# Optimization experiments

Measured on AMD Instinct MI355X. Metric: run time of the kernel, lower is better.

## Reference

```python
import jax, jax.numpy as jnp
import numpy as np

SEQ_LENGTH = 4096
D_MODEL = 2048


def setup_inputs() -> dict:
    key = jax.random.key(0)
    x = jax.random.randint(key, (32, SEQ_LENGTH), 0, 2048)  # [B, S] token ids
    return {"x": x}


def reference(x):
    batch_size = x.shape[0]
    n = 10000.0
    pos = jnp.arange(SEQ_LENGTH, dtype=jnp.float32)[:, None]          # [S, 1]
    i = jnp.arange(D_MODEL // 2, dtype=jnp.float32)[None, :]          # [1, D/2]
    theta = pos / jnp.power(n, (2.0 * i) / D_MODEL)                   # [S, D/2]
    # interleave: even dims = sin, odd dims = cos
    pe = jnp.stack([jnp.sin(theta), jnp.cos(theta)], axis=-1)
    pe = pe.reshape(SEQ_LENGTH, D_MODEL)                              # [S, D]
    return jnp.broadcast_to(pe[None, :, :], (batch_size, SEQ_LENGTH, D_MODEL))
```

## Files before the change

kernel.cpp:

```cpp
#include <hip/hip_runtime.h>
#include <math.h>

#define SEQ_LENGTH 4096
#define D_MODEL   2048
#define BATCH     32
#define TABLE_F4  (SEQ_LENGTH * D_MODEL / 4)
#define TOTAL_F4  (BATCH * TABLE_F4)
#define IT        8

typedef float f4 __attribute__((ext_vector_type(4)));

__global__ __launch_bounds__(256) void PositionalEncoding_54915451847173_kernel(
    float* __restrict__ out) {
    const int base = blockIdx.x * (256 * IT) + threadIdx.x;

    const float c      = -(2.0f / (float)D_MODEL) * 13.28771237954945f;
    const float inv2pi = 0.15915494309189535f;

    #pragma unroll
    for (int it = 0; it < IT; ++it) {
        const int u  = base + it * 256;
        const int t  = u & (TABLE_F4 - 1);
        const int jj = t & (D_MODEL / 4 - 1);
        const int s  = t >> 9;

        const float pos = (float)s;
        const float f0 = __builtin_amdgcn_exp2f(c * (float)(2 * jj));
        const float f1 = __builtin_amdgcn_exp2f(c * (float)(2 * jj + 1));

        const float r0 = __builtin_amdgcn_fractf(pos * (f0 * inv2pi));
        const float r1 = __builtin_amdgcn_fractf(pos * (f1 * inv2pi));

        f4 v;
        v.x = __builtin_amdgcn_sinf(r0);
        v.y = __builtin_amdgcn_cosf(r0);
        v.z = __builtin_amdgcn_sinf(r1);
        v.w = __builtin_amdgcn_cosf(r1);

        ((f4*)out)[u] = v;
    }
}

extern "C" void kernel_launch(void* const* d_in, const int* in_sizes, int n_in,
                              void* d_out, int out_size, void* d_ws, size_t ws_size,
                              hipStream_t stream) {
    (void)d_in; (void)in_sizes; (void)n_in; (void)d_ws; (void)ws_size; (void)out_size;
    float* out = (float*)d_out;
    const int grid = TOTAL_F4 / (256 * IT);
    PositionalEncoding_54915451847173_kernel<<<grid, 256, 0, stream>>>(out);
}
```

Before: 197.2 us.

## Compute each table entry once and stream it to all batch copies

Switches to a persistent grid-stride layout of 2048 blocks. Each thread computes the frequencies for one column once and the sin/cos values for four sequence positions, then writes those four vectors repeatedly across the whole output with a fixed stride. The stride is chosen so the same four values recur across all 32 batch copies. This drops the redundant per-element transcendental work, leaving a purely write-bound store loop. The cost is fewer threads in flight and a serial, non-unrolled store loop per thread.

```diff
diff --git a/kernel.cpp b/kernel.cpp
--- a/kernel.cpp
+++ b/kernel.cpp
@@ -6,38 +6,44 @@
 #define BATCH     32
 #define TABLE_F4  (SEQ_LENGTH * D_MODEL / 4)
 #define TOTAL_F4  (BATCH * TABLE_F4)
-#define IT        8
+#define GRID      2048
+#define STRIDE_F4 (GRID * 256)
+#define NITER     (TOTAL_F4 / STRIDE_F4)
 
 typedef float f4 __attribute__((ext_vector_type(4)));
 
 __global__ __launch_bounds__(256) void PositionalEncoding_54915451847173_kernel(
     float* __restrict__ out) {
-    const int base = blockIdx.x * (256 * IT) + threadIdx.x;
+    const int base = blockIdx.x * 256 + threadIdx.x;
+    const int jj   = base & (D_MODEL / 4 - 1);
+    const int s0   = base >> 9;
 
     const float c      = -(2.0f / (float)D_MODEL) * 13.28771237954945f;
     const float inv2pi = 0.15915494309189535f;
+    const float w0 = __builtin_amdgcn_exp2f(c * (float)(2 * jj)) * inv2pi;
+    const float w1 = __builtin_amdgcn_exp2f(c * (float)(2 * jj + 1)) * inv2pi;
 
+    f4 v[4];
     #pragma unroll
-    for (int it = 0; it < IT; ++it) {
-        const int u  = base + it * 256;
-        const int t  = u & (TABLE_F4 - 1);
-        const int jj = t & (D_MODEL / 4 - 1);
-        const int s  = t >> 9;
+    for (int q = 0; q < 4; ++q) {
+        const float pos = (float)(s0 + 1024 * q);
+        const float r0 = __builtin_amdgcn_fractf(pos * w0);
+        const float r1 = __builtin_amdgcn_fractf(pos * w1);
+        f4 t;
+        t.x = __builtin_amdgcn_sinf(r0);
+        t.y = __builtin_amdgcn_cosf(r0);
+        t.z = __builtin_amdgcn_sinf(r1);
+        t.w = __builtin_amdgcn_cosf(r1);
+        v[q] = t;
+    }
 
-        const float pos = (float)s;
-        const float f0 = __builtin_amdgcn_exp2f(c * (float)(2 * jj));
-        const float f1 = __builtin_amdgcn_exp2f(c * (float)(2 * jj + 1));
-
-        const float r0 = __builtin_amdgcn_fractf(pos * (f0 * inv2pi));
-        const float r1 = __builtin_amdgcn_fractf(pos * (f1 * inv2pi));
-
-        f4 v;
-        v.x = __builtin_amdgcn_sinf(r0);
-        v.y = __builtin_amdgcn_cosf(r0);
-        v.z = __builtin_amdgcn_sinf(r1);
-        v.w = __builtin_amdgcn_cosf(r1);
-
-        ((f4*)out)[u] = v;
+    f4* p = (f4*)out + base;
+    #pragma unroll 1
+    for (int m = 0; m < NITER / 4; ++m) {
+        *p = v[0]; p += STRIDE_F4;
+        *p = v[1]; p += STRIDE_F4;
+        *p = v[2]; p += STRIDE_F4;
+        *p = v[3]; p += STRIDE_F4;
     }
 }
 
@@ -46,6 +52,5 @@
                               hipStream_t stream) {
     (void)d_in; (void)in_sizes; (void)n_in; (void)d_ws; (void)ws_size; (void)out_size;
     float* out = (float*)d_out;
-    const int grid = TOTAL_F4 / (256 * IT);
-    PositionalEncoding_54915451847173_kernel<<<grid, 256, 0, stream>>>(out);
+    PositionalEncoding_54915451847173_kernel<<<GRID, 256, 0, stream>>>(out);
 }
```

After: 249.7 us. +26.6%, slower.
